# Performance work log

Hardware: AMD Instinct MI355X
Metric: run time of the kernel (lower is better)

Reference implementation:

```python
import jax, jax.numpy as jnp
import numpy as np
import math

B, N, H, A, NH = 4, 1024, 1024, 1024, 16
HD = A // NH
MLP_H = int(H * 4.0)          # 4096
FFN = int(MLP_H * 2 / 3)      # 2730 (SwiGLU hidden)
EPS = 1e-6

def _rms(x, w, eps=EPS):
    var = jnp.mean(jnp.square(x), axis=-1, keepdims=True)
    return x * jax.lax.rsqrt(var + eps) * w

def setup_inputs() -> dict:
    key = jax.random.key(0)
    ks = jax.random.split(key, 16)
    def w(k, shape, s=0.02):
        return (jax.random.normal(k, shape) * s).astype(jnp.float32)
    return {
        'x': jax.random.normal(ks[0], (B, N, H), dtype=jnp.float32),
        'c': jax.random.normal(ks[1], (B, H), dtype=jnp.float32),
        'norm1_w': jnp.ones((H,), jnp.float32),
        'compress_w': w(ks[2], (A, H)), 'compress_b': jnp.zeros((A,), jnp.float32),
        'qkv_w': w(ks[3], (3 * A, A)), 'qkv_b': jnp.zeros((3 * A,), jnp.float32),
        'qn_w': jnp.ones((HD,), jnp.float32), 'kn_w': jnp.ones((HD,), jnp.float32),
        'proj_w': w(ks[4], (A, A)), 'proj_b': jnp.zeros((A,), jnp.float32),
        'expand_w': w(ks[5], (H, A)), 'expand_b': jnp.zeros((H,), jnp.float32),
        'norm2_w': jnp.ones((H,), jnp.float32),
        'w12_w': w(ks[6], (2 * FFN, H)), 'w12_b': jnp.zeros((2 * FFN,), jnp.float32),
        'w3_w': w(ks[7], (H, FFN)), 'w3_b': jnp.zeros((H,), jnp.float32),
        'ada_w': w(ks[8], (6 * H, H)), 'ada_b': jnp.zeros((6 * H,), jnp.float32),
    }

def reference(x, c, norm1_w, compress_w, compress_b, qkv_w, qkv_b, qn_w, kn_w,
              proj_w, proj_b, expand_w, expand_b, norm2_w, w12_w, w12_b,
              w3_w, w3_b, ada_w, ada_b):
    # adaLN: SiLU -> Linear -> chunk 6
    ada = jax.nn.silu(c) @ ada_w.T + ada_b                      # [B, 6H]
    sh_msa, sc_msa, g_msa, sh_mlp, sc_mlp, g_mlp = jnp.split(ada, 6, axis=-1)

    def modulate(h, shift, scale):
        return h * (1 + scale[:, None, :]) + shift[:, None, :]

    # --- compact attention branch ---
    h = modulate(_rms(x, norm1_w), sh_msa, sc_msa)              # [B,N,H]
    hc = h @ compress_w.T + compress_b                          # [B,N,A]
    qkv = (hc @ qkv_w.T + qkv_b).reshape(B, N, 3, NH, HD)
    qkv = jnp.transpose(qkv, (2, 0, 3, 1, 4))                   # [3,B,NH,N,HD]
    q, k, v = qkv[0], qkv[1], qkv[2]
    q = _rms(q, qn_w)
    k = _rms(k, kn_w)
    scale = 1.0 / math.sqrt(HD)
    # manual fp32 softmax attention (dropout_p=0 -> identity)
    aw = jnp.einsum('bhnd,bhmd->bhnm', q.astype(jnp.float32),
                    k.astype(jnp.float32)) * scale              # [B,NH,N,N]
    aw = jax.nn.softmax(aw, axis=-1)
    o = jnp.einsum('bhnm,bhmd->bhnd', aw, v)                    # [B,NH,N,HD]
    o = jnp.transpose(o, (0, 2, 1, 3)).reshape(B, N, A)
    o = o @ proj_w.T + proj_b                                   # [B,N,A]
    o = o @ expand_w.T + expand_b                               # [B,N,H]
    x = x + g_msa[:, None, :] * o

    # --- SwiGLU FFN branch ---
    h2 = modulate(_rms(x, norm2_w), sh_mlp, sc_mlp)
    x12 = h2 @ w12_w.T + w12_b                                  # [B,N,2*FFN]
    x1, x2 = jnp.split(x12, 2, axis=-1)
    hid = jax.nn.silu(x1) * x2
    x = x + g_mlp[:, None, :] * (hid @ w3_w.T + w3_b)
    return x
```

## Files before the change

### kernel.cpp

```cpp
#include <hip/hip_runtime.h>
#include <hip/hip_bf16.h>
#include <cstdint>
#include <cstddef>

typedef unsigned short u16;
typedef __bf16 bf16x8 __attribute__((ext_vector_type(8)));
typedef __bf16 bf16x4 __attribute__((ext_vector_type(4)));
typedef short   s16x4 __attribute__((ext_vector_type(4)));
typedef float    f32x4 __attribute__((ext_vector_type(4)));
typedef unsigned short u16x2 __attribute__((ext_vector_type(2)));
typedef unsigned short u16x4 __attribute__((ext_vector_type(4)));
typedef unsigned short u16x8 __attribute__((ext_vector_type(8)));

#define DEVI static __device__ __forceinline__

DEVI float b2f(u16 u){ union{unsigned i; float v;} x; x.i=((unsigned)u)<<16; return x.v; }
DEVI u16 f2b(float f){ union{float v; unsigned i;} x; x.v=f; unsigned r=x.i+0x7FFFu+((x.i>>16)&1u); return (u16)(r>>16); }
DEVI f32x4 mfma16(bf16x8 a, bf16x8 b, f32x4 c){ return __builtin_amdgcn_mfma_f32_16x16x32_bf16(a,b,c,0,0,0); }
DEVI f32x4 mfma16k16(bf16x4 a, bf16x4 b, f32x4 c){
#if __has_builtin(__builtin_amdgcn_mfma_f32_16x16x16_bf16)
  return __builtin_amdgcn_mfma_f32_16x16x16_bf16(a,b,c,0,0,0);
#elif __has_builtin(__builtin_amdgcn_mfma_f32_16x16x16bf16_1k)
  return __builtin_amdgcn_mfma_f32_16x16x16bf16_1k((s16x4)a,(s16x4)b,c,0,0,0);
#else
  asm volatile("v_mfma_f32_16x16x16_bf16 %0, %1, %2, %0" : "+v"(c) : "v"(a), "v"(b));
  return c;
#endif
}
DEVI float fexp2(float x){ return __builtin_amdgcn_exp2f(x); }
DEVI void gload16(const void* g, void* l){
  __builtin_amdgcn_global_load_lds((const __attribute__((address_space(1))) void*)g,
                                   (__attribute__((address_space(3))) void*)l, 16, 0, 0);
}
DEVI float silu_f(float x){ return x/(1.f+__expf(-x)); }

static constexpr size_t OFF_WC   = 0;
static constexpr size_t OFF_WQKV = OFF_WC   + (size_t)1024*1024*2;
static constexpr size_t OFF_WPROJ= OFF_WQKV + (size_t)3072*1024*2;
static constexpr size_t OFF_WEXP = OFF_WPROJ+ (size_t)1024*1024*2;
static constexpr size_t OFF_WW12 = OFF_WEXP + (size_t)1024*1024*2;
static constexpr size_t OFF_WW3  = OFF_WW12 + (size_t)5632*1024*2;
static constexpr size_t OFF_ADA  = OFF_WW3  + (size_t)1024*2752*2;
static constexpr size_t OFF_X2   = OFF_ADA  + (size_t)4*6144*4;
static constexpr size_t OFF_P1   = OFF_X2   + (size_t)4096*1024*4;
static constexpr size_t OFF_H1   = OFF_P1;
static constexpr size_t OFF_HC   = OFF_H1   + (size_t)4096*1024*2;
static constexpr size_t OFF_QKVO = OFF_HC   + (size_t)4096*1024*2;
static constexpr size_t OFF_P2   = OFF_P1   + (size_t)4096*5632*2;
static constexpr size_t OFF_Q    = OFF_P2;
static constexpr size_t OFF_K    = OFF_Q    + (size_t)64*1024*64*2;
static constexpr size_t OFF_VT   = OFF_K    + (size_t)64*1024*64*2;
static constexpr size_t OFF_O    = OFF_VT   + (size_t)64*1024*64*2;
static constexpr size_t OFF_PR   = OFF_O    + (size_t)4096*1024*2;
static constexpr size_t OFF_H2   = OFF_PR   + (size_t)4096*1024*2;
static constexpr size_t OFF_HID  = OFF_P2;

__global__ __launch_bounds__(256) void convert_merged(
    const float* __restrict__ cw, const float* __restrict__ qkvw,
    const float* __restrict__ pw, const float* __restrict__ ew,
    const float* __restrict__ w12w, u16* __restrict__ ws16)
{
  int r = blockIdx.x;
  int c0 = threadIdx.x*4;
  const float* src; u16* dst; long srow; bool valid = true;
  if (r < 1024){ src = cw;   dst = ws16 + OFF_WC/2;   srow = r; }
  else if (r < 4096){ src = qkvw; dst = ws16 + OFF_WQKV/2; srow = r-1024; r -= 1024; }
  else if (r < 5120){ src = pw;   dst = ws16 + OFF_WPROJ/2; srow = r-4096; r -= 4096; }
  else if (r < 6144){ src = ew;   dst = ws16 + OFF_WEXP/2; srow = r-5120; r -= 5120; }
  else {
    int rp = r - 6144;
    int b16 = rp>>4, w = rp&15;
    int p = b16>>1, half = b16&1;
    int sl = p*16 + w;
    valid = sl < 2730;
    srow = (half ? 2730 : 0) + sl;
    src = w12w; dst = ws16 + OFF_WW12/2; r = rp;
  }
  u16x4 o;
#pragma unroll
  for (int j=0;j<4;j++){
    float f = valid ? src[(size_t)srow*1024 + c0 + j] : 0.f;
    o[j] = f2b(f);
  }
  *(u16x4*)&dst[(size_t)r*1024 + c0] = o;
}

__global__ __launch_bounds__(256) void convert_pad(const float* __restrict__ src, u16* __restrict__ dst,
                                                   int R, int C, int Cpad)
{
  int r = blockIdx.y;
  int c0 = (blockIdx.x*256 + threadIdx.x)*4;
  if (c0 >= Cpad) return;
  u16x4 o;
#pragma unroll
  for (int j=0;j<4;j++){
    int cc = c0+j;
    float f = (r < R && cc < C) ? src[(size_t)r*C + cc] : 0.f;
    o[j] = f2b(f);
  }
  *(u16x4*)&dst[(size_t)r*Cpad + c0] = o;
}

__global__ __launch_bounds__(256) void ada_kernel(const float* __restrict__ c,
    const float* __restrict__ aw, const float* __restrict__ ab, float* __restrict__ ada)
{
  __shared__ float s[4][1024];
  int t = threadIdx.x;
#pragma unroll
  for (int i=0;i<16;i++){
    int idx = i*256 + t;
    float cv = c[idx];
    s[idx>>10][idx&1023] = cv/(1.f+__expf(-cv));
  }
  __syncthreads();
  int wid = t>>6, lane = t&63;
  int j = blockIdx.x*4 + wid;
  const f32x4* wp = (const f32x4*)(aw + (size_t)j*1024);
  float a0=0,a1=0,a2=0,a3=0;
#pragma unroll
  for (int i=0;i<4;i++){
    f32x4 wv = wp[i*64 + lane];
    int k0 = (i*64+lane)*4;
#pragma unroll
    for (int e=0;e<4;e++){
      float w = wv[e];
      a0 += w*s[0][k0+e]; a1 += w*s[1][k0+e]; a2 += w*s[2][k0+e]; a3 += w*s[3][k0+e];
    }
  }
#pragma unroll
  for (int mask=1; mask<64; mask<<=1){
    a0 += __shfl_xor(a0, mask); a1 += __shfl_xor(a1, mask);
    a2 += __shfl_xor(a2, mask); a3 += __shfl_xor(a3, mask);
  }
  if (lane==0){
    float bv = ab[j];
    ada[0*6144 + j] = a0 + bv;
    ada[1*6144 + j] = a1 + bv;
    ada[2*6144 + j] = a2 + bv;
    ada[3*6144 + j] = a3 + bv;
  }
}

__global__ __launch_bounds__(256) void rms_mod(const float* __restrict__ x,
    const float* __restrict__ w, const float* __restrict__ ada, int chunkSh,
    u16* __restrict__ out)
{
  int row = blockIdx.x;
  int b = row>>10;
  int t = threadIdx.x;
  int wid = t>>6, lane = t&63;
  f32x4 v = *(const f32x4*)(x + (size_t)row*1024 + t*4);
  float ss = v[0]*v[0]+v[1]*v[1]+v[2]*v[2]+v[3]*v[3];
#pragma unroll
  for (int mask=1; mask<64; mask<<=1) ss += __shfl_xor(ss, mask);
  __shared__ float red[4];
  if (lane==0) red[wid]=ss;
  __syncthreads();
  float rinv = rsqrtf((red[0]+red[1]+red[2]+red[3])*(1.f/1024.f) + 1e-6f);
  int cc = t*4;
  const float* shp = ada + (size_t)b*6144 + (size_t)chunkSh*1024 + cc;
  u16x4 o;
#pragma unroll
  for (int jj=0;jj<4;jj++){
    float val = v[jj]*rinv*w[cc+jj];
    val = val*(1.f+shp[jj+1024]) + shp[jj];
    o[jj] = f2b(val);
  }
  *(u16x4*)&out[(size_t)row*1024 + cc] = o;
}

template<int EPI>
__global__ __launch_bounds__(256) void gemm_dr(
    const u16* __restrict__ A, const u16* __restrict__ Bw, const float* __restrict__ bias,
    int N, int K, int nbias, u16* __restrict__ outb,
    const float* __restrict__ xres, const float* __restrict__ ada, int adaChunk,
    float* __restrict__ outf)
{
  constexpr int RU = 8192;
  __shared__ __align__(16) u16 lds[4*RU];
  int t = threadIdx.x;
  int lane = t&63, w = t>>6;
  int wr = (w>>1)*64, wc = (w&1)*64;
  int lr = lane&15, lg = lane>>4;
  int id = blockIdx.y*8 + blockIdx.x;
  int xcd = id&7, loc = id>>3;
  int bm = xcd*4 + (loc>>3);
  int bn = loc&7;
  int srow = t>>2;
  int schunk = ((t&3) ^ ((t>>3)&3))*8;
  const u16* pA = A  + (size_t)(bm*128 + srow)*K + schunk;
  const u16* pB = Bw + (size_t)(bn*128 + srow)*K + schunk;
  int rp = (lg ^ ((lr>>1)&3))*8;
  int aoff = (wr + lr)*32 + rp;
  int boff = 4096 + (wc + lr)*32 + rp;
  f32x4 acc[4][4] = {};
  int NT = K>>5;

  auto stage = [&](int kt, int slot){
    u16* dst = &lds[slot*RU];
    const u16* sa = pA + (size_t)kt*32;
    const u16* sb = pB + (size_t)kt*32;
    gload16(sa,                dst + t*8);
    gload16(sa + (size_t)64*K, dst + 2048 + t*8);
    gload16(sb,                dst + 4096 + t*8);
    gload16(sb + (size_t)64*K, dst + 6144 + t*8);
  };
  auto compute = [&](int slot){
    const u16* lb = &lds[slot*RU];
    bf16x8 af[4], bfr[4];
#pragma unroll
    for (int m=0;m<4;m++) af[m]  = *(const bf16x8*)&lb[aoff + m*512];
#pragma unroll
    for (int n=0;n<4;n++) bfr[n] = *(const bf16x8*)&lb[boff + n*512];
    __builtin_amdgcn_s_setprio(1);
#pragma unroll
    for (int m=0;m<4;m++)
#pragma unroll
      for (int n=0;n<4;n++)
        acc[m][n] = mfma16(af[m], bfr[n], acc[m][n]);
    __builtin_amdgcn_s_setprio(0);
  };

#pragma unroll
  for (int i=0;i<3;i++) stage(i, i);
  asm volatile("s_waitcnt vmcnt(8)" ::: "memory");
  __builtin_amdgcn_s_barrier();
  __builtin_amdgcn_sched_barrier(0);

  int cur = 0, stg = 3;
  for (int kt=0; kt<NT-3; ++kt){
    stage(kt+3, stg);
    compute(cur);
    asm volatile("s_waitcnt vmcnt(8)" ::: "memory");
    __builtin_amdgcn_s_barrier();
    __builtin_amdgcn_sched_barrier(0);
    cur = (cur==3)?0:cur+1;
    stg = (stg==3)?0:stg+1;
  }
  compute(cur); cur=(cur==3)?0:cur+1;
  asm volatile("s_waitcnt vmcnt(4)" ::: "memory");
  __builtin_amdgcn_s_barrier(); __builtin_amdgcn_sched_barrier(0);
  compute(cur); cur=(cur==3)?0:cur+1;
  asm volatile("s_waitcnt vmcnt(0)" ::: "memory");
  __builtin_amdgcn_s_barrier(); __builtin_amdgcn_sched_barrier(0);
  compute(cur);

#pragma unroll
  for (int n=0;n<4;n++){
    int col = bn*128 + wc + n*16 + lr;
    float bv = (col < nbias) ? bias[col] : 0.f;
#pragma unroll
    for (int m=0;m<4;m++){
      int row0 = bm*128 + wr + m*16 + lg*4;
#pragma unroll
      for (int r=0;r<4;r++){
        int row = row0 + r;
        float v = acc[m][n][r] + bv;
        if constexpr (EPI==0){
          outb[(size_t)row*N + col] = f2b(v);
        } else {
          int bb = row>>10;
          float g = ada[(size_t)bb*6144 + (size_t)adaChunk*1024 + col];
          outf[(size_t)row*1024 + col] = xres[(size_t)row*1024 + col] + g*v;
        }
      }
    }
  }
}

template<int EPI>
__global__ __launch_bounds__(256,2) void gemm_dp2(
    const u16* __restrict__ A, const u16* __restrict__ Bw, const float* __restrict__ bias,
    int N, int K, int nbias, u16* __restrict__ outb)
{
  constexpr int AU = 128*32;
  constexpr int RU = AU + 256*32;
  __shared__ __align__(16) u16 lds[3*RU];
  int t = threadIdx.x;
  int lane = t&63, w = t>>6;
  int wr = w>>1, wc = w&1;
  int lr = lane&15, lg = lane>>4;
  int nbn = gridDim.x;
  int id = blockIdx.y*nbn + blockIdx.x;
  int chunk = (nbn*(int)gridDim.y)>>3;
  int g = (id&7)*chunk + (id>>3);
  int bm = 0;
  while (g >= nbn){ g -= nbn; ++bm; }
  int bn = g;
  int schunk = ((t&3) ^ ((t>>3)&3))*8;
  const u16* pA = A  + (size_t)(bm*128 + (t>>2))*K + schunk;
  const u16* pB = Bw + (size_t)(bn*256 + (t>>2))*K + schunk;
  int rsw  = (lg ^ ((lr>>1)&3))*8;
  int aoff = (wr*64 + lr)*32 + rsw;
  int boff = AU + (wc*128 + lr)*32 + rsw;
  f32x4 acc[4][8] = {};
  int NT = K>>5;

  auto stage = [&](int kt, int rg){
    u16* dst = &lds[rg*RU];
    const u16* sa = pA + (size_t)kt*32;
    const u16* sb = pB + (size_t)kt*32;
    gload16(sa,                  dst + t*8);
    gload16(sa + (size_t)64*K,   dst + 2048 + t*8);
#pragma unroll
    for (int i=0;i<4;i++)
      gload16(sb + (size_t)(i*64)*K, dst + AU + i*2048 + t*8);
  };

  stage(0, 0);
  stage(1, 1);
  asm volatile("s_waitcnt vmcnt(6)" ::: "memory");
  __builtin_amdgcn_s_barrier();
  __builtin_amdgcn_sched_barrier(0);

  int cur = 0, stg = 2;
  for (int kt=0; kt<NT; ++kt){
    const u16* lb = &lds[cur*RU];
    if (kt+2 < NT) stage(kt+2, stg);
    bf16x8 af[4], bfr[8];
#pragma unroll
    for (int mf=0;mf<4;mf++) af[mf] = *(const bf16x8*)&lb[aoff + mf*512];
#pragma unroll
    for (int nf=0;nf<8;nf++) bfr[nf] = *(const bf16x8*)&lb[boff + nf*512];
    __builtin_amdgcn_s_setprio(1);
#pragma unroll
    for (int mf=0;mf<4;mf++)
#pragma unroll
      for (int nf=0;nf<8;nf++)
        acc[mf][nf] = mfma16(af[mf], bfr[nf], acc[mf][nf]);
    __builtin_amdgcn_s_setprio(0);
    if (kt+2 < NT){
      asm volatile("s_waitcnt vmcnt(6)" ::: "memory");
    } else if (kt+1 < NT){
      asm volatile("s_waitcnt vmcnt(0)" ::: "memory");
    }
    if (kt+1 < NT){
      __builtin_amdgcn_s_barrier();
      __builtin_amdgcn_sched_barrier(0);
    }
    cur = (cur==2)?0:cur+1;
    stg = (stg==2)?0:stg+1;
  }
  if constexpr (EPI==0){
#pragma unroll
    for (int nf=0;nf<8;nf++){
      int col = bn*256 + wc*128 + nf*16 + lr;
      float bv = (col < nbias) ? bias[col] : 0.f;
#pragma unroll
      for (int mf=0; mf<4; mf++){
        int row0 = bm*128 + wr*64 + mf*16 + lg*4;
#pragma unroll
        for (int r=0;r<4;r++)
          outb[(size_t)(row0+r)*N + col] = f2b(acc[mf][nf][r] + bv);
      }
    }
  } else {
#pragma unroll
    for (int nf=0;nf<8;nf+=2){
      int p = bn*8 + wc*4 + (nf>>1);
      int P = p*16 + lr;
      bool vP = (P < 2730);
      float b1 = vP ? bias[P] : 0.f;
      float b2 = vP ? bias[2730+P] : 0.f;
#pragma unroll
      for (int mf=0; mf<4; mf++){
        int row0 = bm*128 + wr*64 + mf*16 + lg*4;
#pragma unroll
        for (int r=0;r<4;r++){
          float x1 = acc[mf][nf][r] + b1;
          float x2 = acc[mf][nf+1][r] + b2;
          if (vP) outb[(size_t)(row0+r)*2752 + P] = f2b(silu_f(x1)*x2);
        }
      }
    }
  }
}

__global__ __launch_bounds__(256) void repack_qkv(const u16* __restrict__ qkvO,
    const float* __restrict__ qnw, const float* __restrict__ knw,
    u16* __restrict__ qO, u16* __restrict__ kO, u16* __restrict__ vO)
{
  __shared__ u16 ldsv[64][64];
  int bh = blockIdx.y, b = bh>>4, h = bh&15;
  int n0 = blockIdx.x*64;
  int t = threadIdx.x;
  int nr = t>>2, qd = (t&3)*16;
  const u16* rowp = qkvO + (size_t)(b*1024 + n0 + nr)*3072;
  {
    u16x8 a0 = *(const u16x8*)(rowp + h*64 + qd);
    u16x8 a1 = *(const u16x8*)(rowp + h*64 + qd + 8);
    float f[16]; float ss=0;
#pragma unroll
    for (int jj=0;jj<8;jj++){ f[jj]=b2f(a0[jj]); f[8+jj]=b2f(a1[jj]); }
#pragma unroll
    for (int jj=0;jj<16;jj++) ss += f[jj]*f[jj];
    ss += __shfl_xor(ss,1); ss += __shfl_xor(ss,2);
    float rinv = rsqrtf(ss*(1.f/64.f)+1e-6f)*0.125f*1.44269504089f;
    u16x8 o0,o1;
#pragma unroll
    for (int jj=0;jj<8;jj++){ o0[jj]=f2b(f[jj]*rinv*qnw[qd+jj]); o1[jj]=f2b(f[8+jj]*rinv*qnw[qd+8+jj]); }
    u16* dst = qO + ((size_t)bh*1024 + n0 + nr)*64 + qd;
    *(u16x8*)dst = o0; *(u16x8*)(dst+8) = o1;
  }
  {
    u16x8 a0 = *(const u16x8*)(rowp + 1024 + h*64 + qd);
    u16x8 a1 = *(const u16x8*)(rowp + 1024 + h*64 + qd + 8);
    float f[16]; float ss=0;
#pragma unroll
    for (int jj=0;jj<8;jj++){ f[jj]=b2f(a0[jj]); f[8+jj]=b2f(a1[jj]); }
#pragma unroll
    for (int jj=0;jj<16;jj++) ss += f[jj]*f[jj];
    ss += __shfl_xor(ss,1); ss += __shfl_xor(ss,2);
    float rinv = rsqrtf(ss*(1.f/64.f)+1e-6f);
    u16x8 o0,o1;
#pragma unroll
    for (int jj=0;jj<8;jj++){ o0[jj]=f2b(f[jj]*rinv*knw[qd+jj]); o1[jj]=f2b(f[8+jj]*rinv*knw[qd+8+jj]); }
    int t16 = (n0 + nr)>>4, lrk = nr&15;
    {
      int d0 = qd, c = d0>>5, lg = (d0>>3)&3;
      *(u16x8*)(kO + (size_t)bh*65536 + ((size_t)(t16*2+c)*64 + lg*16 + lrk)*8) = o0;
    }
    {
      int d0 = qd+8, c = d0>>5, lg = (d0>>3)&3;
      *(u16x8*)(kO + (size_t)bh*65536 + ((size_t)(t16*2+c)*64 + lg*16 + lrk)*8) = o1;
    }
  }
  {
    u16x8 a0 = *(const u16x8*)(rowp + 2048 + h*64 + qd);
    u16x8 a1 = *(const u16x8*)(rowp + 2048 + h*64 + qd + 8);
#pragma unroll
    for (int jj=0;jj<8;jj++){ ldsv[qd+jj][nr] = a0[jj]; ldsv[qd+8+jj][nr] = a1[jj]; }
  }
  __syncthreads();
  {
    int d = t>>2, ns = (t&3)*16;
    int tt = d>>4, lrv = d&15;
    int m = (n0 + ns)>>5;
    int hf = (ns>>4)&1;
    u16* basep = vO + (size_t)bh*65536 + ((size_t)(m*4+tt)*64 + lrv)*8 + hf*4;
#pragma unroll
    for (int g=0; g<4; ++g){
      u16x4 wv4 = { ldsv[d][ns+g*4], ldsv[d][ns+g*4+1], ldsv[d][ns+g*4+2], ldsv[d][ns+g*4+3] };
      *(u16x4*)(basep + (size_t)g*128) = wv4;
    }
  }
}

__global__ __launch_bounds__(512) void attn_fwd(const u16* __restrict__ qO,
    const u16* __restrict__ kO, const u16* __restrict__ vO, u16* __restrict__ o)
{
  __shared__ __align__(16) float obuf[4][64][16];
  __shared__ __align__(16) float mlb[4][2][2][16];
  int bh = blockIdx.y, b = bh>>4, h = bh&15;
  int w = threadIdx.x>>6, lane = threadIdx.x&63;
  int pair = w>>1, half = w&1;
  int lr = lane&15, lg = lane>>4;
  int q0 = blockIdx.x*64 + pair*16;
  const u16* qp = qO + ((size_t)bh*1024 + q0 + lr)*64 + lg*8;
  bf16x8 qf0 = *(const bf16x8*)qp;
  bf16x8 qf1 = *(const bf16x8*)(qp + 32);
  const u16* kb = kO + (size_t)bh*65536 + (size_t)half*32768 + (size_t)lane*8;
  const u16* vb = vO + (size_t)bh*65536 + (size_t)half*32768 + (size_t)lane*8;
  f32x4 oacc[4] = {};
  float mrun = -3.0e38f, lrun = 0.f;
  for (int it=0; it<16; ++it){
    const u16* kp = kb + (size_t)it*4096;
    bf16x8 k00 = *(const bf16x8*)(kp);
    bf16x8 k01 = *(const bf16x8*)(kp + 512);
    bf16x8 k10 = *(const bf16x8*)(kp + 1024);
    bf16x8 k11 = *(const bf16x8*)(kp + 1536);
    f32x4 s0 = {}, s1 = {};
    s0 = mfma16(k00, qf0, s0); s0 = mfma16(k01, qf1, s0);
    s1 = mfma16(k10, qf0, s1); s1 = mfma16(k11, qf1, s1);
    const u16* vp = vb + (size_t)it*2048;
    bf16x8 vv[4];
#pragma unroll
    for (int tt=0;tt<4;tt++) vv[tt] = *(const bf16x8*)(vp + tt*512);
    float pm = fmaxf(fmaxf(fmaxf(s0[0],s0[1]),fmaxf(s0[2],s0[3])),
                     fmaxf(fmaxf(s1[0],s1[1]),fmaxf(s1[2],s1[3])));
    pm = fmaxf(pm, __shfl_xor(pm, 16));
    pm = fmaxf(pm, __shfl_xor(pm, 32));
    if (__any(pm > mrun + 8.f)){
      float mnew = fmaxf(mrun, pm);
      float alpha = fexp2(mrun - mnew);
      mrun = mnew;
      lrun *= alpha;
      float ar[4];
#pragma unroll
      for (int r=0;r<4;r++) ar[r] = __shfl(alpha, lg*4 + r);
#pragma unroll
      for (int tt=0;tt<4;tt++)
#pragma unroll
        for (int r=0;r<4;r++) oacc[tt][r] *= ar[r];
    }
    float p0[4], p1[4]; float ls = 0.f;
#pragma unroll
    for (int r=0;r<4;r++){ p0[r]=fexp2(s0[r]-mrun); p1[r]=fexp2(s1[r]-mrun); ls += p0[r]+p1[r]; }
    ls += __shfl_xor(ls, 16); ls += __shfl_xor(ls, 32);
    lrun += ls;
    bf16x4 pa0, pa1;
#pragma unroll
    for (int r=0;r<4;r++){ pa0[r] = (__bf16)p0[r]; pa1[r] = (__bf16)p1[r]; }
#pragma unroll
    for (int tt=0;tt<4;tt++){
      bf16x4* vh = (bf16x4*)&vv[tt];
      oacc[tt] = mfma16k16(pa0, vh[0], oacc[tt]);
      oacc[tt] = mfma16k16(pa1, vh[1], oacc[tt]);
    }
  }
  if (lg==0){ mlb[pair][half][0][lr] = mrun; mlb[pair][half][1][lr] = lrun; }
  __syncthreads();
  f32x4 m0 = *(const f32x4*)&mlb[pair][0][0][lg*4];
  f32x4 l0 = *(const f32x4*)&mlb[pair][0][1][lg*4];
  f32x4 m1 = *(const f32x4*)&mlb[pair][1][0][lg*4];
  f32x4 l1 = *(const f32x4*)&mlb[pair][1][1][lg*4];
  f32x4 fh;
#pragma unroll
  for (int r=0;r<4;r++){
    float m = fmaxf(m0[r], m1[r]);
    float e0 = fexp2(m0[r]-m), e1 = fexp2(m1[r]-m);
    float li = 1.f/(l0[r]*e0 + l1[r]*e1);
    fh[r] = (half ? e1 : e0)*li;
  }
  if (half==1){
#pragma unroll
    for (int tt=0;tt<4;tt++){
      f32x4 tv;
#pragma unroll
      for (int r=0;r<4;r++) tv[r] = oacc[tt][r]*fh[r];
      *(f32x4*)&obuf[pair][lane][tt*4] = tv;
    }
  }
  __syncthreads();
  if (half==0){
#pragma unroll
    for (int tt=0;tt<4;tt++){
      f32x4 p = *(const f32x4*)&obuf[pair][lane][tt*4];
#pragma unroll
      for (int r=0;r<4;r++){
        int row = (b<<10) + q0 + lg*4 + r;
        int col = h*64 + tt*16 + lr;
        o[(size_t)row*1024 + col] = f2b(oacc[tt][r]*fh[r] + p[r]);
      }
    }
  }
}

extern "C" void kernel_launch(void* const* d_in, const int* in_sizes, int n_in,
                              void* d_out, int out_size, void* d_ws, size_t ws_size,
                              hipStream_t stream)
{
  (void)in_sizes; (void)n_in; (void)out_size; (void)ws_size;
  const float* x    = (const float*)d_in[0];
  const float* c    = (const float*)d_in[1];
  const float* n1w  = (const float*)d_in[2];
  const float* cw   = (const float*)d_in[3];
  const float* cb   = (const float*)d_in[4];
  const float* qkvw = (const float*)d_in[5];
  const float* qkvb = (const float*)d_in[6];
  const float* qnw  = (const float*)d_in[7];
  const float* knw  = (const float*)d_in[8];
  const float* pw   = (const float*)d_in[9];
  const float* pb   = (const float*)d_in[10];
  const float* ew   = (const float*)d_in[11];
  const float* eb   = (const float*)d_in[12];
  const float* n2w  = (const float*)d_in[13];
  const float* w12w = (const float*)d_in[14];
  const float* w12b = (const float*)d_in[15];
  const float* w3w  = (const float*)d_in[16];
  const float* w3b  = (const float*)d_in[17];
  const float* adaw = (const float*)d_in[18];
  const float* adab = (const float*)d_in[19];
  float* out = (float*)d_out;
  char* ws = (char*)d_ws;
  auto U = [&](size_t off){ return (u16*)(ws + off); };
  auto F = [&](size_t off){ return (float*)(ws + off); };

  convert_merged<<<11776, 256, 0, stream>>>(cw, qkvw, pw, ew, w12w, (u16*)ws);
  convert_pad<<<dim3(3,1024), 256, 0, stream>>>(w3w, U(OFF_WW3), 1024, 2730, 2752);

  ada_kernel<<<1536, 256, 0, stream>>>(c, adaw, adab, F(OFF_ADA));

  rms_mod<<<4096, 256, 0, stream>>>(x, n1w, F(OFF_ADA), 0, U(OFF_H1));
  gemm_dr<0><<<dim3(8,32), 256, 0, stream>>>(U(OFF_H1), U(OFF_WC), cb, 1024, 1024, 1024, U(OFF_HC), nullptr, nullptr, 0, nullptr);
  gemm_dp2<0><<<dim3(12,32), 256, 0, stream>>>(U(OFF_HC), U(OFF_WQKV), qkvb, 3072, 1024, 3072, U(OFF_QKVO));
  repack_qkv<<<dim3(16,64), 256, 0, stream>>>(U(OFF_QKVO), qnw, knw, U(OFF_Q), U(OFF_K), U(OFF_VT));
  attn_fwd<<<dim3(16,64), 512, 0, stream>>>(U(OFF_Q), U(OFF_K), U(OFF_VT), U(OFF_O));
  gemm_dr<0><<<dim3(8,32), 256, 0, stream>>>(U(OFF_O), U(OFF_WPROJ), pb, 1024, 1024, 1024, U(OFF_PR), nullptr, nullptr, 0, nullptr);
  gemm_dr<1><<<dim3(8,32), 256, 0, stream>>>(U(OFF_PR), U(OFF_WEXP), eb, 1024, 1024, 1024, nullptr, x, F(OFF_ADA), 2, F(OFF_X2));

  rms_mod<<<4096, 256, 0, stream>>>(F(OFF_X2), n2w, F(OFF_ADA), 3, U(OFF_H2));
  gemm_dp2<2><<<dim3(22,32), 256, 0, stream>>>(U(OFF_H2), U(OFF_WW12), w12b, 5632, 1024, 5460, U(OFF_HID));
  gemm_dr<1><<<dim3(8,32), 256, 0, stream>>>(U(OFF_HID), U(OFF_WW3), w3b, 1024, 2752, 1024, nullptr, F(OFF_X2), F(OFF_ADA), 5, out);
}
```

Measured before the change: 278.2 us.

## Replace 128x256 GEMM with 256x256 tile, 8 waves, quad-buffered interleaved staging

```diff
diff --git a/kernel.cpp b/kernel.cpp
--- a/kernel.cpp
+++ b/kernel.cpp
@@ -269,16 +269,15 @@
 }
 
 template<int EPI>
-__global__ __launch_bounds__(256,2) void gemm_dp2(
+__global__ __launch_bounds__(512) void gemm_q4(
     const u16* __restrict__ A, const u16* __restrict__ Bw, const float* __restrict__ bias,
     int N, int K, int nbias, u16* __restrict__ outb)
 {
-  constexpr int AU = 128*32;
-  constexpr int RU = AU + 256*32;
-  __shared__ __align__(16) u16 lds[3*RU];
+  constexpr int BU = 16384;
+  __shared__ __align__(16) u16 lds[4*BU];
   int t = threadIdx.x;
   int lane = t&63, w = t>>6;
-  int wr = w>>1, wc = w&1;
+  int wr = w>>2, wc = w&3;
   int lr = lane&15, lg = lane>>4;
   int nbn = gridDim.x;
   int id = blockIdx.y*nbn + blockIdx.x;
@@ -287,68 +286,104 @@
   int bm = 0;
   while (g >= nbn){ g -= nbn; ++bm; }
   int bn = g;
+  int srow = t>>2;
   int schunk = ((t&3) ^ ((t>>3)&3))*8;
-  const u16* pA = A  + (size_t)(bm*128 + (t>>2))*K + schunk;
-  const u16* pB = Bw + (size_t)(bn*256 + (t>>2))*K + schunk;
-  int rsw  = (lg ^ ((lr>>1)&3))*8;
-  int aoff = (wr*64 + lr)*32 + rsw;
-  int boff = AU + (wc*128 + lr)*32 + rsw;
-  f32x4 acc[4][8] = {};
+  const u16* pA = A  + (size_t)(bm*256 + srow)*K + schunk;
+  const u16* pB = Bw + (size_t)(bn*256 + srow)*K + schunk;
+  int rp = (lg ^ ((lr>>1)&3))*8;
+  f32x4 acc[8][4] = {};
   int NT = K>>5;
 
-  auto stage = [&](int kt, int rg){
-    u16* dst = &lds[rg*RU];
-    const u16* sa = pA + (size_t)kt*32;
-    const u16* sb = pB + (size_t)kt*32;
-    gload16(sa,                  dst + t*8);
-    gload16(sa + (size_t)64*K,   dst + 2048 + t*8);
-#pragma unroll
-    for (int i=0;i<4;i++)
-      gload16(sb + (size_t)(i*64)*K, dst + AU + i*2048 + t*8);
+  auto stageK = [&](int kt, int kind){
+    int buf = kt&3;
+    const u16* src = ((kind<2)? pA : pB) + (size_t)((kind&1)*128)*K + (size_t)kt*32;
+    u16* dst = &lds[buf*BU + ((kind>=2)?8192:0) + (kind&1)*4096 + t*8];
+    gload16(src, dst);
   };
-
-  stage(0, 0);
-  stage(1, 1);
-  asm volatile("s_waitcnt vmcnt(6)" ::: "memory");
+  auto readA = [&](int buf, int mf)->bf16x8 {
+    int R = wr*128 + mf*16 + lr;
+    return *(const bf16x8*)&lds[buf*BU + R*32 + rp];
+  };
+  auto readB = [&](int buf, int nf)->bf16x8 {
+    int R = wc*64 + nf*16 + lr;
+    return *(const bf16x8*)&lds[buf*BU + 8192 + R*32 + rp];
+  };
+
+#pragma unroll
+  for (int k=0;k<4;k++) stageK(0,k);
+#pragma unroll
+  for (int k=0;k<4;k++) stageK(1,k);
+  asm volatile("s_waitcnt vmcnt(4)" ::: "memory");
   __builtin_amdgcn_s_barrier();
   __builtin_amdgcn_sched_barrier(0);
 
-  int cur = 0, stg = 2;
   for (int kt=0; kt<NT; ++kt){
-    const u16* lb = &lds[cur*RU];
-    if (kt+2 < NT) stage(kt+2, stg);
-    bf16x8 af[4], bfr[8];
-#pragma unroll
-    for (int mf=0;mf<4;mf++) af[mf] = *(const bf16x8*)&lb[aoff + mf*512];
-#pragma unroll
-    for (int nf=0;nf<8;nf++) bfr[nf] = *(const bf16x8*)&lb[boff + nf*512];
+    int buf = kt&3;
+    bool pre = (kt+2 < NT);
+    bf16x8 af[4], bfr[2];
+#pragma unroll
+    for (int mf=0;mf<4;mf++) af[mf] = readA(buf, mf);
+    bfr[0] = readB(buf, 0); bfr[1] = readB(buf, 1);
+    if (pre) stageK(kt+2, 0);
+    asm volatile("s_waitcnt lgkmcnt(0)" ::: "memory");
+    __builtin_amdgcn_sched_barrier(0);
     __builtin_amdgcn_s_setprio(1);
 #pragma unroll
     for (int mf=0;mf<4;mf++)
 #pragma unroll
-      for (int nf=0;nf<8;nf++)
+      for (int nf=0;nf<2;nf++)
         acc[mf][nf] = mfma16(af[mf], bfr[nf], acc[mf][nf]);
     __builtin_amdgcn_s_setprio(0);
-    if (kt+2 < NT){
-      asm volatile("s_waitcnt vmcnt(6)" ::: "memory");
-    } else if (kt+1 < NT){
-      asm volatile("s_waitcnt vmcnt(0)" ::: "memory");
-    }
+    bfr[0] = readB(buf, 2); bfr[1] = readB(buf, 3);
+    if (pre) stageK(kt+2, 1);
+    asm volatile("s_waitcnt lgkmcnt(0)" ::: "memory");
+    __builtin_amdgcn_sched_barrier(0);
+    __builtin_amdgcn_s_setprio(1);
+#pragma unroll
+    for (int mf=0;mf<4;mf++)
+#pragma unroll
+      for (int nf=0;nf<2;nf++)
+        acc[mf][2+nf] = mfma16(af[mf], bfr[nf], acc[mf][2+nf]);
+    __builtin_amdgcn_s_setprio(0);
+#pragma unroll
+    for (int mf=0;mf<4;mf++) af[mf] = readA(buf, 4+mf);
+    if (pre) stageK(kt+2, 2);
+    asm volatile("s_waitcnt lgkmcnt(0)" ::: "memory");
+    __builtin_amdgcn_sched_barrier(0);
+    __builtin_amdgcn_s_setprio(1);
+#pragma unroll
+    for (int mf=0;mf<4;mf++)
+#pragma unroll
+      for (int nf=0;nf<2;nf++)
+        acc[4+mf][2+nf] = mfma16(af[mf], bfr[nf], acc[4+mf][2+nf]);
+    __builtin_amdgcn_s_setprio(0);
+    bfr[0] = readB(buf, 0); bfr[1] = readB(buf, 1);
+    if (pre) stageK(kt+2, 3);
+    asm volatile("s_waitcnt lgkmcnt(0)" ::: "memory");
+    __builtin_amdgcn_sched_barrier(0);
+    __builtin_amdgcn_s_setprio(1);
+#pragma unroll
+    for (int mf=0;mf<4;mf++)
+#pragma unroll
+      for (int nf=0;nf<2;nf++)
+        acc[4+mf][nf] = mfma16(af[mf], bfr[nf], acc[4+mf][nf]);
+    __builtin_amdgcn_s_setprio(0);
     if (kt+1 < NT){
+      if (kt+2 < NT) asm volatile("s_waitcnt vmcnt(4)" ::: "memory");
+      else           asm volatile("s_waitcnt vmcnt(0)" ::: "memory");
       __builtin_amdgcn_s_barrier();
       __builtin_amdgcn_sched_barrier(0);
     }
-    cur = (cur==2)?0:cur+1;
-    stg = (stg==2)?0:stg+1;
-  }
+  }
+
   if constexpr (EPI==0){
 #pragma unroll
-    for (int nf=0;nf<8;nf++){
-      int col = bn*256 + wc*128 + nf*16 + lr;
+    for (int nf=0;nf<4;nf++){
+      int col = bn*256 + wc*64 + nf*16 + lr;
       float bv = (col < nbias) ? bias[col] : 0.f;
 #pragma unroll
-      for (int mf=0; mf<4; mf++){
-        int row0 = bm*128 + wr*64 + mf*16 + lg*4;
+      for (int mf=0; mf<8; mf++){
+        int row0 = bm*256 + wr*128 + mf*16 + lg*4;
 #pragma unroll
         for (int r=0;r<4;r++)
           outb[(size_t)(row0+r)*N + col] = f2b(acc[mf][nf][r] + bv);
@@ -356,15 +391,15 @@
     }
   } else {
 #pragma unroll
-    for (int nf=0;nf<8;nf+=2){
-      int p = bn*8 + wc*4 + (nf>>1);
+    for (int nf=0;nf<4;nf+=2){
+      int p = bn*8 + wc*2 + (nf>>1);
       int P = p*16 + lr;
       bool vP = (P < 2730);
       float b1 = vP ? bias[P] : 0.f;
       float b2 = vP ? bias[2730+P] : 0.f;
 #pragma unroll
-      for (int mf=0; mf<4; mf++){
-        int row0 = bm*128 + wr*64 + mf*16 + lg*4;
+      for (int mf=0; mf<8; mf++){
+        int row0 = bm*256 + wr*128 + mf*16 + lg*4;
 #pragma unroll
         for (int r=0;r<4;r++){
           float x1 = acc[mf][nf][r] + b1;
@@ -583,13 +618,13 @@
 
   rms_mod<<<4096, 256, 0, stream>>>(x, n1w, F(OFF_ADA), 0, U(OFF_H1));
   gemm_dr<0><<<dim3(8,32), 256, 0, stream>>>(U(OFF_H1), U(OFF_WC), cb, 1024, 1024, 1024, U(OFF_HC), nullptr, nullptr, 0, nullptr);
-  gemm_dp2<0><<<dim3(12,32), 256, 0, stream>>>(U(OFF_HC), U(OFF_WQKV), qkvb, 3072, 1024, 3072, U(OFF_QKVO));
+  gemm_q4<0><<<dim3(12,16), 512, 0, stream>>>(U(OFF_HC), U(OFF_WQKV), qkvb, 3072, 1024, 3072, U(OFF_QKVO));
   repack_qkv<<<dim3(16,64), 256, 0, stream>>>(U(OFF_QKVO), qnw, knw, U(OFF_Q), U(OFF_K), U(OFF_VT));
   attn_fwd<<<dim3(16,64), 512, 0, stream>>>(U(OFF_Q), U(OFF_K), U(OFF_VT), U(OFF_O));
   gemm_dr<0><<<dim3(8,32), 256, 0, stream>>>(U(OFF_O), U(OFF_WPROJ), pb, 1024, 1024, 1024, U(OFF_PR), nullptr, nullptr, 0, nullptr);
   gemm_dr<1><<<dim3(8,32), 256, 0, stream>>>(U(OFF_PR), U(OFF_WEXP), eb, 1024, 1024, 1024, nullptr, x, F(OFF_ADA), 2, F(OFF_X2));
 
   rms_mod<<<4096, 256, 0, stream>>>(F(OFF_X2), n2w, F(OFF_ADA), 3, U(OFF_H2));
-  gemm_dp2<2><<<dim3(22,32), 256, 0, stream>>>(U(OFF_H2), U(OFF_WW12), w12b, 5632, 1024, 5460, U(OFF_HID));
+  gemm_q4<2><<<dim3(22,16), 512, 0, stream>>>(U(OFF_H2), U(OFF_WW12), w12b, 5632, 1024, 5460, U(OFF_HID));
   gemm_dr<1><<<dim3(8,32), 256, 0, stream>>>(U(OFF_HID), U(OFF_WW3), w3b, 1024, 2752, 1024, nullptr, F(OFF_X2), F(OFF_ADA), 5, out);
 }
```

Result: slower. 284.2 us (+2.1%).

## Fold proj and expand linear layers into one precomputed weight matrix

Applied to the files above, without the earlier changes.

```diff
diff --git a/kernel.cpp b/kernel.cpp
--- a/kernel.cpp
+++ b/kernel.cpp
@@ -52,6 +52,9 @@
 static constexpr size_t OFF_VT   = OFF_K    + (size_t)64*1024*64*2;
 static constexpr size_t OFF_O    = OFF_VT   + (size_t)64*1024*64*2;
 static constexpr size_t OFF_PR   = OFF_O    + (size_t)4096*1024*2;
+static constexpr size_t OFF_PWT  = OFF_PR;
+static constexpr size_t OFF_WPE  = OFF_PR   + (size_t)1024*1024*2;
+static constexpr size_t OFF_BEP  = OFF_PR   + (size_t)2*1024*1024*2;
 static constexpr size_t OFF_H2   = OFF_PR   + (size_t)4096*1024*2;
 static constexpr size_t OFF_HID  = OFF_P2;
 
@@ -101,6 +104,43 @@
   *(u16x4*)&dst[(size_t)r*Cpad + c0] = o;
 }
 
+__global__ __launch_bounds__(256) void tconv(const float* __restrict__ src, u16* __restrict__ dst,
+                                             int R, int C)
+{
+  __shared__ u16 tile[64][65];
+  int r0 = blockIdx.y*64, c0 = blockIdx.x*64;
+  int t = threadIdx.x;
+  int r = t>>2, cs = (t&3)*16;
+  const float* sp = src + (size_t)(r0+r)*C + c0 + cs;
+#pragma unroll
+  for (int j=0;j<16;j++) tile[r][cs+j] = f2b(sp[j]);
+  __syncthreads();
+  int cc = t>>2, rs = (t&3)*16;
+  u16x8 o0, o1;
+#pragma unroll
+  for (int j=0;j<8;j++){ o0[j] = tile[rs+j][cc]; o1[j] = tile[rs+8+j][cc]; }
+  u16* dp = dst + (size_t)(c0+cc)*R + r0 + rs;
+  *(u16x8*)dp = o0; *(u16x8*)(dp+8) = o1;
+}
+
+__global__ __launch_bounds__(256) void matvec(const float* __restrict__ W, const float* __restrict__ v,
+                                              const float* __restrict__ b, float* __restrict__ out)
+{
+  int row = blockIdx.x*4 + (threadIdx.x>>6);
+  int lane = threadIdx.x&63;
+  const f32x4* wp = (const f32x4*)(W + (size_t)row*1024);
+  const f32x4* vp = (const f32x4*)v;
+  float s = 0.f;
+#pragma unroll
+  for (int i=0;i<4;i++){
+    f32x4 wv = wp[i*64+lane], vv = vp[i*64+lane];
+    s += wv[0]*vv[0]+wv[1]*vv[1]+wv[2]*vv[2]+wv[3]*vv[3];
+  }
+#pragma unroll
+  for (int mask=1; mask<64; mask<<=1) s += __shfl_xor(s, mask);
+  if (lane==0) out[row] = s + b[row];
+}
+
 __global__ __launch_bounds__(256) void ada_kernel(const float* __restrict__ c,
     const float* __restrict__ aw, const float* __restrict__ ab, float* __restrict__ ada)
 {
@@ -182,10 +222,13 @@
   int lane = t&63, w = t>>6;
   int wr = (w>>1)*64, wc = (w&1)*64;
   int lr = lane&15, lg = lane>>4;
-  int id = blockIdx.y*8 + blockIdx.x;
-  int xcd = id&7, loc = id>>3;
-  int bm = xcd*4 + (loc>>3);
-  int bn = loc&7;
+  int bm, bn;
+  if (gridDim.y == 32){
+    int id = blockIdx.y*8 + blockIdx.x;
+    int xcd = id&7, loc = id>>3;
+    bm = xcd*4 + (loc>>3);
+    bn = loc&7;
+  } else { bm = blockIdx.y; bn = blockIdx.x; }
   int srow = t>>2;
   int schunk = ((t&3) ^ ((t>>3)&3))*8;
   const u16* pA = A  + (size_t)(bm*128 + srow)*K + schunk;
@@ -578,6 +621,9 @@
 
   convert_merged<<<11776, 256, 0, stream>>>(cw, qkvw, pw, ew, w12w, (u16*)ws);
   convert_pad<<<dim3(3,1024), 256, 0, stream>>>(w3w, U(OFF_WW3), 1024, 2730, 2752);
+  tconv<<<dim3(16,16), 256, 0, stream>>>(pw, U(OFF_PWT), 1024, 1024);
+  gemm_dr<0><<<dim3(8,8), 256, 0, stream>>>(U(OFF_WEXP), U(OFF_PWT), nullptr, 1024, 1024, 0, U(OFF_WPE), nullptr, nullptr, 0, nullptr);
+  matvec<<<256, 256, 0, stream>>>(ew, pb, eb, F(OFF_BEP));
 
   ada_kernel<<<1536, 256, 0, stream>>>(c, adaw, adab, F(OFF_ADA));
 
@@ -586,8 +632,7 @@
   gemm_dp2<0><<<dim3(12,32), 256, 0, stream>>>(U(OFF_HC), U(OFF_WQKV), qkvb, 3072, 1024, 3072, U(OFF_QKVO));
   repack_qkv<<<dim3(16,64), 256, 0, stream>>>(U(OFF_QKVO), qnw, knw, U(OFF_Q), U(OFF_K), U(OFF_VT));
   attn_fwd<<<dim3(16,64), 512, 0, stream>>>(U(OFF_Q), U(OFF_K), U(OFF_VT), U(OFF_O));
-  gemm_dr<0><<<dim3(8,32), 256, 0, stream>>>(U(OFF_O), U(OFF_WPROJ), pb, 1024, 1024, 1024, U(OFF_PR), nullptr, nullptr, 0, nullptr);
-  gemm_dr<1><<<dim3(8,32), 256, 0, stream>>>(U(OFF_PR), U(OFF_WEXP), eb, 1024, 1024, 1024, nullptr, x, F(OFF_ADA), 2, F(OFF_X2));
+  gemm_dr<1><<<dim3(8,32), 256, 0, stream>>>(U(OFF_O), U(OFF_WPE), F(OFF_BEP), 1024, 1024, 1024, nullptr, x, F(OFF_ADA), 2, F(OFF_X2));
 
   rms_mod<<<4096, 256, 0, stream>>>(F(OFF_X2), n2w, F(OFF_ADA), 3, U(OFF_H2));
   gemm_dp2<2><<<dim3(22,32), 256, 0, stream>>>(U(OFF_H2), U(OFF_WW12), w12b, 5632, 1024, 5460, U(OFF_HID));
```

Result: no change. 281.3 us (+1.1%).
